# Kernel tuning notes

Measured on AMD Instinct MI355X. Metric: run time of the kernel, lower is better.

Reference implementation:

```python
import jax, jax.numpy as jnp
import numpy as np
from jax import lax

B, T, C = 32, 4096, 128
CLAMP_LO, CLAMP_HI = 1e-4, 1.0 - 1e-4
LOGIT_ALPHA0 = 0.0                 # logit(0.5)
LOGIT_BETA0 = float(np.log(0.1 / 0.9))  # logit(0.1)


def setup_inputs() -> dict:
    key = jax.random.key(0)
    x = jax.random.normal(key, (B, T, C), dtype=jnp.float32)
    logit_alpha = jnp.full((C,), LOGIT_ALPHA0, dtype=jnp.float32)
    logit_beta = jnp.full((C,), LOGIT_BETA0, dtype=jnp.float32)
    return {"x": x, "logit_alpha": logit_alpha, "logit_beta": logit_beta}


def reference(x, logit_alpha, logit_beta):
    # Holt level+slope exponential smoothing; output is the level series.
    a = jnp.clip(jax.nn.sigmoid(logit_alpha), CLAMP_LO, CLAMP_HI).astype(x.dtype)  # [C]
    b = jnp.clip(jax.nn.sigmoid(logit_beta), CLAMP_LO, CLAMP_HI).astype(x.dtype)   # [C]

    L0 = x[:, 0, :]                       # [B, C]
    slope0 = jnp.zeros_like(L0)

    def step(carry, xt):
        L_prev, slope = carry
        pred = L_prev + slope
        L = pred + a * (xt - pred)
        slope = slope + b * (L - L_prev - slope)
        return (L, slope), L

    xs = jnp.moveaxis(x[:, 1:, :], 1, 0)  # [T-1, B, C], time-major for scan
    _, Ls = lax.scan(step, (L0, slope0), xs)
    out = jnp.concatenate([L0[:, None, :], jnp.moveaxis(Ls, 0, 1)], axis=1)  # [B, T, C]
    return out
```

## Files before the change

### kernel.cpp

```cpp
#include <hip/hip_runtime.h>
#include <math.h>


#define B_ 32
#define T_ 4096
#define C_ 128
#define K_ 64
#define S_ (T_ / K_)

__device__ __forceinline__ float sig_clamp(float z) {
    float s = 1.0f / (1.0f + expf(-z));
    return fminf(fmaxf(s, 1.0e-4f), 1.0f - 1.0e-4f);
}

__global__ __launch_bounds__(C_) void p1_chunk_offsets(
        const float* __restrict__ x,
        const float* __restrict__ logit_alpha,
        const float* __restrict__ logit_beta,
        float2* __restrict__ w) {
    const int blk = blockIdx.x;
    const int b = blk / K_;
    const int k = blk % K_;
    const int c = threadIdx.x;

    const float a  = sig_clamp(logit_alpha[c]);
    const float bb = sig_clamp(logit_beta[c]);

    const float* xp = x + ((size_t)b * T_ + (size_t)k * S_) * C_ + c;

    float L, sl;
    int t0;
    if (k == 0) {
        L = xp[0];
        sl = 0.0f;
        xp += C_;
        t0 = 1;
    } else {
        L = 0.0f;
        sl = 0.0f;
        t0 = 0;
    }
    #pragma unroll 8
    for (int t = t0; t < S_; ++t) {
        const float xv = *xp;
        xp += C_;
        const float pred = L + sl;
        const float Ln = pred + a * (xv - pred);
        sl = sl + bb * (Ln - L - sl);
        L = Ln;
    }
    w[((size_t)b * K_ + k) * C_ + c] = make_float2(L, sl);
}

__global__ __launch_bounds__(256) void p2_chunk_scan(
        const float2* __restrict__ w,
        const float* __restrict__ logit_alpha,
        const float* __restrict__ logit_beta,
        float2* __restrict__ sstart) {
    const int tid = blockIdx.x * blockDim.x + threadIdx.x;
    if (tid >= B_ * C_) return;
    const int b = tid / C_;
    const int c = tid % C_;

    const float a  = sig_clamp(logit_alpha[c]);
    const float bb = sig_clamp(logit_beta[c]);

    float m00 = 1.0f - a, m01 = 1.0f - a;
    float m10 = -a * bb,  m11 = 1.0f - a * bb;
    #pragma unroll
    for (int i = 0; i < 6; ++i) {
        const float n00 = m00 * m00 + m01 * m10;
        const float n01 = m00 * m01 + m01 * m11;
        const float n10 = m10 * m00 + m11 * m10;
        const float n11 = m10 * m01 + m11 * m11;
        m00 = n00; m01 = n01; m10 = n10; m11 = n11;
    }

    const size_t base = (size_t)b * K_ * C_ + c;
    float2 s = w[base];
    #pragma unroll 8
    for (int k = 1; k < K_; ++k) {
        sstart[base + (size_t)k * C_] = s;
        const float2 wk = w[base + (size_t)k * C_];
        const float L  = m00 * s.x + m01 * s.y + wk.x;
        const float sl = m10 * s.x + m11 * s.y + wk.y;
        s = make_float2(L, sl);
    }
}

__global__ __launch_bounds__(C_) void p3_emit(
        const float* __restrict__ x,
        const float* __restrict__ logit_alpha,
        const float* __restrict__ logit_beta,
        const float2* __restrict__ sstart,
        float* __restrict__ out) {
    const int blk = blockIdx.x;
    const int b = blk / K_;
    const int k = blk % K_;
    const int c = threadIdx.x;

    const float a  = sig_clamp(logit_alpha[c]);
    const float bb = sig_clamp(logit_beta[c]);

    const size_t off = ((size_t)b * T_ + (size_t)k * S_) * C_ + c;
    const float* xp = x + off;
    float* op = out + off;

    float L, sl;
    int t0;
    if (k == 0) {
        L = xp[0];
        sl = 0.0f;
        op[0] = L;
        xp += C_; op += C_;
        t0 = 1;
    } else {
        const float2 s = sstart[((size_t)b * K_ + k) * C_ + c];
        L = s.x; sl = s.y;
        t0 = 0;
    }
    #pragma unroll 8
    for (int t = t0; t < S_; ++t) {
        const float xv = *xp;
        xp += C_;
        const float pred = L + sl;
        const float Ln = pred + a * (xv - pred);
        sl = sl + bb * (Ln - L - sl);
        L = Ln;
        *op = L;
        op += C_;
    }
}

__global__ void seq_fallback(
        const float* __restrict__ x,
        const float* __restrict__ logit_alpha,
        const float* __restrict__ logit_beta,
        float* __restrict__ out) {
    const int tid = blockIdx.x * blockDim.x + threadIdx.x;
    if (tid >= B_ * C_) return;
    const int b = tid / C_;
    const int c = tid % C_;
    const float a  = sig_clamp(logit_alpha[c]);
    const float bb = sig_clamp(logit_beta[c]);
    const float* xp = x + (size_t)b * T_ * C_ + c;
    float* op = out + (size_t)b * T_ * C_ + c;
    float L = xp[0], sl = 0.0f;
    op[0] = L;
    for (int t = 1; t < T_; ++t) {
        const float xv = xp[(size_t)t * C_];
        const float pred = L + sl;
        const float Ln = pred + a * (xv - pred);
        sl = sl + bb * (Ln - L - sl);
        L = Ln;
        op[(size_t)t * C_] = L;
    }
}

extern "C" void kernel_launch(void* const* d_in, const int* in_sizes, int n_in,
                              void* d_out, int out_size, void* d_ws, size_t ws_size,
                              hipStream_t stream) {
    const float* x  = (const float*)d_in[0];
    const float* la = (const float*)d_in[1];
    const float* lb = (const float*)d_in[2];
    float* out = (float*)d_out;

    const size_t n_state = (size_t)B_ * K_ * C_;
    const size_t need = 2 * n_state * sizeof(float2);

    if (ws_size >= need) {
        float2* w      = (float2*)d_ws;
        float2* sstart = w + n_state;
        p1_chunk_offsets<<<B_ * K_, C_, 0, stream>>>(x, la, lb, w);
        p2_chunk_scan<<<(B_ * C_ + 255) / 256, 256, 0, stream>>>(w, la, lb, sstart);
        p3_emit<<<B_ * K_, C_, 0, stream>>>(x, la, lb, sstart, out);
    } else {
        seq_fallback<<<(B_ * C_ + 255) / 256, 256, 0, stream>>>(x, la, lb, out);
    }
}
```

Before: 135.2 us.

## Fuse chunk-carry scan into emit kernel and process two channels per thread

Removes the separate sequential chunk-scan kernel. Each emit chunk now recomputes its own starting state by scanning the preceding chunk summaries of its batch, and blocks are launched in reverse order so that long-prefix chunks start first. Threads now handle two channels through float2 loads and stores with float4 state summaries, and the step is rewritten with an FMA-based slope update. This trades redundant prefix work, up to 63 float4 loads per thread, for one fewer launch and less workspace traffic.

```diff
diff --git a/kernel.cpp b/kernel.cpp
--- a/kernel.cpp
+++ b/kernel.cpp
@@ -7,128 +7,129 @@
 #define C_ 128
 #define K_ 64
 #define S_ (T_ / K_)
+#define C2 (C_ / 2)
+#define NCHUNK (B_ * K_)
 
 __device__ __forceinline__ float sig_clamp(float z) {
     float s = 1.0f / (1.0f + expf(-z));
     return fminf(fmaxf(s, 1.0e-4f), 1.0f - 1.0e-4f);
 }
 
-__global__ __launch_bounds__(C_) void p1_chunk_offsets(
+#define STEP(xv0, xv1)                                   \
+    {                                                    \
+        const float p0 = L0 + sl0;                       \
+        const float p1 = L1 + sl1;                       \
+        const float g0 = a0 * ((xv0) - p0);              \
+        const float g1 = a1 * ((xv1) - p1);              \
+        L0 = p0 + g0;  sl0 = fmaf(b0, g0, sl0);          \
+        L1 = p1 + g1;  sl1 = fmaf(b1, g1, sl1);          \
+    }
+
+__global__ __launch_bounds__(256) void p1_offsets(
         const float* __restrict__ x,
         const float* __restrict__ logit_alpha,
         const float* __restrict__ logit_beta,
-        float2* __restrict__ w) {
-    const int blk = blockIdx.x;
-    const int b = blk / K_;
-    const int k = blk % K_;
-    const int c = threadIdx.x;
+        float4* __restrict__ w) {
+    const int tid = threadIdx.x & 63;
+    const int chunk = blockIdx.x * 4 + (threadIdx.x >> 6);
+    const int b = chunk >> 6;
+    const int k = chunk & (K_ - 1);
 
-    const float a  = sig_clamp(logit_alpha[c]);
-    const float bb = sig_clamp(logit_beta[c]);
+    const float2 la2 = ((const float2*)logit_alpha)[tid];
+    const float2 lb2 = ((const float2*)logit_beta)[tid];
+    const float a0 = sig_clamp(la2.x), a1 = sig_clamp(la2.y);
+    const float b0 = sig_clamp(lb2.x), b1 = sig_clamp(lb2.y);
 
-    const float* xp = x + ((size_t)b * T_ + (size_t)k * S_) * C_ + c;
+    const float2* xp = (const float2*)x + ((size_t)b * T_ + (size_t)k * S_) * C2 + tid;
 
-    float L, sl;
+    float L0, sl0 = 0.0f, L1, sl1 = 0.0f;
     int t0;
     if (k == 0) {
-        L = xp[0];
-        sl = 0.0f;
-        xp += C_;
+        const float2 v = xp[0];
+        L0 = v.x; L1 = v.y;
+        xp += C2;
         t0 = 1;
     } else {
-        L = 0.0f;
-        sl = 0.0f;
+        L0 = 0.0f; L1 = 0.0f;
         t0 = 0;
     }
     #pragma unroll 8
     for (int t = t0; t < S_; ++t) {
-        const float xv = *xp;
-        xp += C_;
-        const float pred = L + sl;
-        const float Ln = pred + a * (xv - pred);
-        sl = sl + bb * (Ln - L - sl);
-        L = Ln;
+        const float2 xv = *xp;
+        xp += C2;
+        STEP(xv.x, xv.y);
     }
-    w[((size_t)b * K_ + k) * C_ + c] = make_float2(L, sl);
+    w[(size_t)chunk * 64 + tid] = make_float4(L0, sl0, L1, sl1);
 }
 
-__global__ __launch_bounds__(256) void p2_chunk_scan(
-        const float2* __restrict__ w,
-        const float* __restrict__ logit_alpha,
-        const float* __restrict__ logit_beta,
-        float2* __restrict__ sstart) {
-    const int tid = blockIdx.x * blockDim.x + threadIdx.x;
-    if (tid >= B_ * C_) return;
-    const int b = tid / C_;
-    const int c = tid % C_;
-
-    const float a  = sig_clamp(logit_alpha[c]);
-    const float bb = sig_clamp(logit_beta[c]);
-
-    float m00 = 1.0f - a, m01 = 1.0f - a;
-    float m10 = -a * bb,  m11 = 1.0f - a * bb;
-    #pragma unroll
-    for (int i = 0; i < 6; ++i) {
-        const float n00 = m00 * m00 + m01 * m10;
-        const float n01 = m00 * m01 + m01 * m11;
-        const float n10 = m10 * m00 + m11 * m10;
-        const float n11 = m10 * m01 + m11 * m11;
-        m00 = n00; m01 = n01; m10 = n10; m11 = n11;
-    }
-
-    const size_t base = (size_t)b * K_ * C_ + c;
-    float2 s = w[base];
-    #pragma unroll 8
-    for (int k = 1; k < K_; ++k) {
-        sstart[base + (size_t)k * C_] = s;
-        const float2 wk = w[base + (size_t)k * C_];
-        const float L  = m00 * s.x + m01 * s.y + wk.x;
-        const float sl = m10 * s.x + m11 * s.y + wk.y;
-        s = make_float2(L, sl);
-    }
-}
-
-__global__ __launch_bounds__(C_) void p3_emit(
+__global__ __launch_bounds__(256) void p2_emit(
         const float* __restrict__ x,
         const float* __restrict__ logit_alpha,
         const float* __restrict__ logit_beta,
-        const float2* __restrict__ sstart,
+        const float4* __restrict__ w,
         float* __restrict__ out) {
-    const int blk = blockIdx.x;
-    const int b = blk / K_;
-    const int k = blk % K_;
-    const int c = threadIdx.x;
+    const int tid = threadIdx.x & 63;
+    const int chunk = (NCHUNK - 1) - (blockIdx.x * 4 + (threadIdx.x >> 6));
+    const int b = chunk >> 6;
+    const int k = chunk & (K_ - 1);
 
-    const float a  = sig_clamp(logit_alpha[c]);
-    const float bb = sig_clamp(logit_beta[c]);
+    const float2 la2 = ((const float2*)logit_alpha)[tid];
+    const float2 lb2 = ((const float2*)logit_beta)[tid];
+    const float a0 = sig_clamp(la2.x), a1 = sig_clamp(la2.y);
+    const float b0 = sig_clamp(lb2.x), b1 = sig_clamp(lb2.y);
 
-    const size_t off = ((size_t)b * T_ + (size_t)k * S_) * C_ + c;
-    const float* xp = x + off;
-    float* op = out + off;
+    const size_t off = ((size_t)b * T_ + (size_t)k * S_) * C2 + tid;
+    const float2* xp = (const float2*)x + off;
+    float2* op = (float2*)out + off;
 
-    float L, sl;
+    float L0, sl0, L1, sl1;
     int t0;
     if (k == 0) {
-        L = xp[0];
-        sl = 0.0f;
-        op[0] = L;
-        xp += C_; op += C_;
+        const float2 v = xp[0];
+        L0 = v.x; L1 = v.y; sl0 = 0.0f; sl1 = 0.0f;
+        op[0] = make_float2(L0, L1);
+        xp += C2; op += C2;
         t0 = 1;
     } else {
-        const float2 s = sstart[((size_t)b * K_ + k) * C_ + c];
-        L = s.x; sl = s.y;
+        float m00_0 = 1.0f - a0, m01_0 = 1.0f - a0;
+        float m10_0 = -a0 * b0,  m11_0 = 1.0f - a0 * b0;
+        float m00_1 = 1.0f - a1, m01_1 = 1.0f - a1;
+        float m10_1 = -a1 * b1,  m11_1 = 1.0f - a1 * b1;
+        #pragma unroll
+        for (int i = 0; i < 6; ++i) {
+            float n00 = m00_0 * m00_0 + m01_0 * m10_0;
+            float n01 = m00_0 * m01_0 + m01_0 * m11_0;
+            float n10 = m10_0 * m00_0 + m11_0 * m10_0;
+            float n11 = m10_0 * m01_0 + m11_0 * m11_0;
+            m00_0 = n00; m01_0 = n01; m10_0 = n10; m11_0 = n11;
+            n00 = m00_1 * m00_1 + m01_1 * m10_1;
+            n01 = m00_1 * m01_1 + m01_1 * m11_1;
+            n10 = m10_1 * m00_1 + m11_1 * m10_1;
+            n11 = m10_1 * m01_1 + m11_1 * m11_1;
+            m00_1 = n00; m01_1 = n01; m10_1 = n10; m11_1 = n11;
+        }
+        const float4* wp = w + (size_t)b * K_ * 64 + tid;
+        float4 s = wp[0];
+        #pragma unroll 4
+        for (int j = 1; j < k; ++j) {
+            const float4 wj = wp[(size_t)j * 64];
+            const float nx = m00_0 * s.x + m01_0 * s.y + wj.x;
+            const float ny = m10_0 * s.x + m11_0 * s.y + wj.y;
+            const float nz = m00_1 * s.z + m01_1 * s.w + wj.z;
+            const float nw = m10_1 * s.z + m11_1 * s.w + wj.w;
+            s = make_float4(nx, ny, nz, nw);
+        }
+        L0 = s.x; sl0 = s.y; L1 = s.z; sl1 = s.w;
         t0 = 0;
     }
+
     #pragma unroll 8
     for (int t = t0; t < S_; ++t) {
-        const float xv = *xp;
-        xp += C_;
-        const float pred = L + sl;
-        const float Ln = pred + a * (xv - pred);
-        sl = sl + bb * (Ln - L - sl);
-        L = Ln;
-        *op = L;
-        op += C_;
+        const float2 xv = *xp;
+        xp += C2;
+        STEP(xv.x, xv.y);
+        *op = make_float2(L0, L1);
+        op += C2;
     }
 }
 
@@ -141,19 +142,19 @@
     if (tid >= B_ * C_) return;
     const int b = tid / C_;
     const int c = tid % C_;
-    const float a  = sig_clamp(logit_alpha[c]);
-    const float bb = sig_clamp(logit_beta[c]);
+    const float a0 = sig_clamp(logit_alpha[c]);
+    const float b0 = sig_clamp(logit_beta[c]);
     const float* xp = x + (size_t)b * T_ * C_ + c;
     float* op = out + (size_t)b * T_ * C_ + c;
-    float L = xp[0], sl = 0.0f;
-    op[0] = L;
+    float L0 = xp[0], sl0 = 0.0f;
+    op[0] = L0;
     for (int t = 1; t < T_; ++t) {
         const float xv = xp[(size_t)t * C_];
-        const float pred = L + sl;
-        const float Ln = pred + a * (xv - pred);
-        sl = sl + bb * (Ln - L - sl);
-        L = Ln;
-        op[(size_t)t * C_] = L;
+        const float p0 = L0 + sl0;
+        const float g0 = a0 * (xv - p0);
+        L0 = p0 + g0;
+        sl0 = fmaf(b0, g0, sl0);
+        op[(size_t)t * C_] = L0;
     }
 }
 
@@ -165,15 +166,12 @@
     const float* lb = (const float*)d_in[2];
     float* out = (float*)d_out;
 
-    const size_t n_state = (size_t)B_ * K_ * C_;
-    const size_t need = 2 * n_state * sizeof(float2);
+    const size_t need = (size_t)NCHUNK * 64 * sizeof(float4);
 
     if (ws_size >= need) {
-        float2* w      = (float2*)d_ws;
-        float2* sstart = w + n_state;
-        p1_chunk_offsets<<<B_ * K_, C_, 0, stream>>>(x, la, lb, w);
-        p2_chunk_scan<<<(B_ * C_ + 255) / 256, 256, 0, stream>>>(w, la, lb, sstart);
-        p3_emit<<<B_ * K_, C_, 0, stream>>>(x, la, lb, sstart, out);
+        float4* w = (float4*)d_ws;
+        p1_offsets<<<NCHUNK / 4, 256, 0, stream>>>(x, la, lb, w);
+        p2_emit<<<NCHUNK / 4, 256, 0, stream>>>(x, la, lb, w, out);
     } else {
         seq_fallback<<<(B_ * C_ + 255) / 256, 256, 0, stream>>>(x, la, lb, out);
     }
```

After: 130.4 us. 3.5% less time.
